# Optimization experiments

Measured on AMD Instinct MI355X. Metric: run time of the kernel, lower is better.

The kernel has to match this reference:

```python
import jax, jax.numpy as jnp
import numpy as np

DIM = 192
NUM_HEADS = 6
KSZ = 7
MLP_RATIO = 4.0
LEVELS = 8
EPS = 1e-5


def layernorm(x, w, b):
    mu = jnp.mean(x, axis=-1, keepdims=True)
    var = jnp.mean(jnp.square(x - mu), axis=-1, keepdims=True)
    return (x - mu) * jax.lax.rsqrt(var + EPS) * w + b


def na2d(x, qkv_w, qkv_b, proj_w, proj_b, rpb):
    # Neighborhood attention 2D with relative position bias (NATTEN semantics:
    # window of KSZ x KSZ keys per query, clamped to stay inside the image).
    B, H, W, C = x.shape
    nh, hd = NUM_HEADS, C // NUM_HEADS
    scale = hd ** -0.5
    qkv = (x @ qkv_w.T + qkv_b).reshape(B, H, W, 3, nh, hd)
    q = qkv[..., 0, :, :] * scale  # [B,H,W,nh,hd]
    k = qkv[..., 1, :, :]
    v = qkv[..., 2, :, :]

    si = jnp.clip(jnp.arange(H) - KSZ // 2, 0, H - KSZ)
    idx_i = si[:, None] + jnp.arange(KSZ)  # [H,KSZ] row indices of each window
    sj = jnp.clip(jnp.arange(W) - KSZ // 2, 0, W - KSZ)
    idx_j = sj[:, None] + jnp.arange(KSZ)  # [W,KSZ]

    def gather_win(t):  # [B,H,W,nh,hd] -> [B,H,KSZ,W,KSZ,nh,hd]
        t = jnp.take(t, idx_i.reshape(-1), axis=1).reshape(B, H, KSZ, W, nh, hd)
        t = jnp.take(t, idx_j.reshape(-1), axis=3).reshape(B, H, KSZ, W, KSZ, nh, hd)
        return t

    kw = gather_win(k)
    vw = gather_win(v)

    # scores over the KSZ x KSZ neighborhood
    scores = jnp.einsum('bxynd,bxiyjnd->bxynij', q, kw)  # [B,H,W,nh,KSZ,KSZ]

    # relative position bias: rpb is [nh, 2K-1, 2K-1]
    rel_i = idx_i - jnp.arange(H)[:, None] + (KSZ - 1)  # [H,KSZ] in [0,2K-2]
    rel_j = idx_j - jnp.arange(W)[:, None] + (KSZ - 1)  # [W,KSZ]
    bias = rpb[:, rel_i][:, :, :, rel_j]  # [nh,H,KSZ,W,KSZ]
    scores = scores + bias.transpose(1, 3, 0, 2, 4)[None]

    attn = jax.nn.softmax(scores.reshape(B, H, W, nh, KSZ * KSZ), axis=-1)
    attn = attn.reshape(B, H, W, nh, KSZ, KSZ)
    out = jnp.einsum('bxynij,bxiyjnd->bxynd', attn, vw).reshape(B, H, W, C)
    return out @ proj_w.T + proj_b


def setup_inputs() -> dict:
    key = jax.random.key(0)
    ks = jax.random.split(key, 8)
    C = DIM
    hidden = int(C * MLP_RATIO)
    init = lambda k, shape: (jax.random.normal(k, shape, dtype=jnp.float32) * 0.02)
    return {
        'x': jax.random.normal(ks[0], (1, 128, 128, C), dtype=jnp.float32),
        'qkv_w': init(ks[1], (3 * C, C)),
        'qkv_b': jnp.zeros((3 * C,), jnp.float32),
        'proj_w': init(ks[2], (C, C)),
        'proj_b': jnp.zeros((C,), jnp.float32),
        'rpb': init(ks[3], (NUM_HEADS, 2 * KSZ - 1, 2 * KSZ - 1)),
        'ln1_w': jnp.ones((C,), jnp.float32),
        'ln1_b': jnp.zeros((C,), jnp.float32),
        'ln2_w': jnp.ones((C,), jnp.float32),
        'ln2_b': jnp.zeros((C,), jnp.float32),
        'fc1_w': init(ks[4], (hidden, C)),
        'fc1_b': jnp.zeros((hidden,), jnp.float32),
        'fc2_w': init(ks[5], (C, hidden)),
        'fc2_b': jnp.zeros((C,), jnp.float32),
        'gamma1': jnp.ones((LEVELS, C), jnp.float32),
        'gamma2': jnp.ones((LEVELS, C), jnp.float32),
        'quality': 4,
    }


def reference(x, qkv_w, qkv_b, proj_w, proj_b, rpb, ln1_w, ln1_b, ln2_w, ln2_b,
              fc1_w, fc1_b, fc2_w, fc2_b, gamma1, gamma2, quality):
    # eval-mode quality gating; quality is an integer so l = quality % 1 == 0
    s = int(quality) - 1
    g1 = jnp.abs(gamma1[s])
    g2 = jnp.abs(gamma2[s])

    shortcut = x
    h = layernorm(x, ln1_w, ln1_b)
    a = na2d(h, qkv_w, qkv_b, proj_w, proj_b, rpb)
    x = shortcut + g1 * a
    h2 = layernorm(x, ln2_w, ln2_b)
    m = jax.nn.gelu(h2 @ fc1_w.T + fc1_b, approximate=False) @ fc2_w.T + fc2_b
    x = x + g2 * m
    return x
```

## Files before the change

kernel.cpp:

```cpp
#include <hip/hip_runtime.h>
#include <hip/hip_bf16.h>
#include <math.h>

#define DIM 192
#define NHD 6
#define HD 32
#define KSZ 7
#define HID 768
#define IMH 128
#define IMW 128
#define NPIX (IMH*IMW)
#define WIN 14
#define KPAD 40

typedef __attribute__((ext_vector_type(8))) short short8;
typedef __attribute__((ext_vector_type(4))) float f32x4;

#define LDS_SYNC() do { \
    asm volatile("s_waitcnt lgkmcnt(0)" ::: "memory"); \
    __builtin_amdgcn_sched_barrier(0); \
    __builtin_amdgcn_s_barrier(); } while (0)

__global__ __launch_bounds__(256) void cvt_w(
    const float* __restrict__ qw, __hip_bfloat16* __restrict__ dq)
{
    int idx = blockIdx.x * 1024 + threadIdx.x * 4;
    float4 v4 = *(const float4*)(qw + idx);
    union { ushort4 u; __hip_bfloat16 h[4]; } o;
    o.h[0] = __float2bfloat16(v4.x); o.h[1] = __float2bfloat16(v4.y);
    o.h[2] = __float2bfloat16(v4.z); o.h[3] = __float2bfloat16(v4.w);
    *(ushort4*)&dq[idx] = o.u;
}

__device__ __forceinline__ void gl_lds16(const void* g, void* l) {
    __builtin_amdgcn_global_load_lds(
        (const __attribute__((address_space(1))) void*)g,
        (__attribute__((address_space(3))) void*)l, 16, 0, 0);
}

__device__ __forceinline__ short8 cvt8(float4 a, float4 b) {
    union { short8 v; __hip_bfloat16 h[8]; } u;
    u.h[0] = __float2bfloat16(a.x); u.h[1] = __float2bfloat16(a.y);
    u.h[2] = __float2bfloat16(a.z); u.h[3] = __float2bfloat16(a.w);
    u.h[4] = __float2bfloat16(b.x); u.h[5] = __float2bfloat16(b.y);
    u.h[6] = __float2bfloat16(b.z); u.h[7] = __float2bfloat16(b.w);
    return u.v;
}

__device__ __forceinline__ void stage_rows(const __hip_bfloat16* __restrict__ src,
                                           char* ldsbase, int wave, int lane) {
    int c0 = wave * 96 + lane;
    int r0 = c0 / 24, k0 = c0 - r0 * 24;
    gl_lds16(src + (size_t)r0 * DIM + ((k0 ^ (r0 & 7)) * 8), ldsbase + (wave * 96) * 16);
    int c1 = wave * 96 + 64 + (lane & 31);
    int r1 = c1 / 24, k1 = c1 - r1 * 24;
    if (lane < 32)
        gl_lds16(src + (size_t)r1 * DIM + ((k1 ^ (r1 & 7)) * 8), ldsbase + (wave * 96 + 64) * 16);
}
__device__ __forceinline__ void stage_w2(const __hip_bfloat16* __restrict__ W2, int ch,
                                         char* ldsbase, int wave, int lane) {
    int i0 = wave * 96 + lane;
    int r0 = i0 >> 3, o0 = i0 & 7;
    gl_lds16(W2 + (size_t)r0 * HID + ch * 64 + ((o0 ^ (r0 & 7)) * 8), ldsbase + (wave * 96) * 16);
    int i1 = wave * 96 + 64 + (lane & 31);
    int r1 = i1 >> 3, o1 = i1 & 7;
    if (lane < 32)
        gl_lds16(W2 + (size_t)r1 * HID + ch * 64 + ((o1 ^ (r1 & 7)) * 8), ldsbase + (wave * 96 + 64) * 16);
}

__global__ __launch_bounds__(256, 2) void qkv_ln_gemm(
    const float* __restrict__ x, const float* __restrict__ lnw, const float* __restrict__ lnb,
    const __hip_bfloat16* __restrict__ W, const float* __restrict__ bias,
    float* __restrict__ qb, __hip_bfloat16* __restrict__ kb, __hip_bfloat16* __restrict__ vb)
{
    __shared__ __hip_bfloat16 As[32 * 192];
    __shared__ __hip_bfloat16 Ws2[2][64 * 192];
    int tid = threadIdx.x;
    int wave = tid >> 6, lane = tid & 63;
    int q = lane >> 4, col = lane & 15;
    int wm = (wave >> 1) * 16, wn = (wave & 1) * 32;
    int m0 = blockIdx.x * 32;

    auto stageW = [&](int ch, int buf) {
        #pragma unroll
        for (int i = 0; i < 6; i++) {
            int c = i * 256 + tid;
            int r = c / 24, kc = c - r * 24;
            gl_lds16(W + (size_t)(ch * 64 + r) * DIM + ((kc ^ (r & 7)) * 8),
                     (char*)&Ws2[buf][0] + (i * 256 + wave * 64) * 16);
        }
    };

    stageW(0, 0);

    {
        int row = tid >> 3, sub = tid & 7;
        const float4* xr = (const float4*)(x + (size_t)(m0 + row) * DIM + sub * 24);
        float4 xa[6];
        float s = 0.f;
        #pragma unroll
        for (int i = 0; i < 6; i++) {
            xa[i] = xr[i];
            s += xa[i].x + xa[i].y + xa[i].z + xa[i].w;
        }
        s += __shfl_xor(s, 1); s += __shfl_xor(s, 2); s += __shfl_xor(s, 4);
        float mu = s * (1.0f / DIM);
        float qs = 0.f;
        #pragma unroll
        for (int i = 0; i < 6; i++) {
            float a = xa[i].x - mu, b = xa[i].y - mu, c = xa[i].z - mu, d = xa[i].w - mu;
            qs += a * a + b * b + c * c + d * d;
        }
        qs += __shfl_xor(qs, 1); qs += __shfl_xor(qs, 2); qs += __shfl_xor(qs, 4);
        float rstd = rsqrtf(qs * (1.0f / DIM) + 1e-5f);
        const float4* wv = (const float4*)(lnw + sub * 24);
        const float4* bv = (const float4*)(lnb + sub * 24);
        #pragma unroll
        for (int j = 0; j < 3; j++) {
            float4 v0 = xa[j * 2], v1 = xa[j * 2 + 1];
            float4 w0 = wv[j * 2], w1 = wv[j * 2 + 1];
            float4 b0 = bv[j * 2], b1 = bv[j * 2 + 1];
            float4 o0, o1;
            o0.x = (v0.x - mu) * rstd * w0.x + b0.x;
            o0.y = (v0.y - mu) * rstd * w0.y + b0.y;
            o0.z = (v0.z - mu) * rstd * w0.z + b0.z;
            o0.w = (v0.w - mu) * rstd * w0.w + b0.w;
            o1.x = (v1.x - mu) * rstd * w1.x + b1.x;
            o1.y = (v1.y - mu) * rstd * w1.y + b1.y;
            o1.z = (v1.z - mu) * rstd * w1.z + b1.z;
            o1.w = (v1.w - mu) * rstd * w1.w + b1.w;
            int oct = sub * 3 + j;
            *(short8*)&As[row * 192 + ((oct ^ (row & 7)) * 8)] = cvt8(o0, o1);
        }
    }
    asm volatile("s_waitcnt lgkmcnt(0)" ::: "memory");
    __builtin_amdgcn_sched_barrier(0);
    __builtin_amdgcn_s_barrier();

    short8 af[6];
    {
        int rA = wm + col;
        #pragma unroll
        for (int ks = 0; ks < 6; ks++)
            af[ks] = *(const short8*)&As[rA * 192 + (((ks * 4 + q) ^ (rA & 7)) * 8)];
    }

    for (int ch = 0; ch < 9; ch++) {
        if (ch < 8) {
            stageW(ch + 1, (ch + 1) & 1);
            asm volatile("s_waitcnt vmcnt(6)" ::: "memory");
        } else {
            asm volatile("s_waitcnt vmcnt(0)" ::: "memory");
        }
        __builtin_amdgcn_s_barrier();
        const __hip_bfloat16* wsb = &Ws2[ch & 1][0];
        f32x4 acc[2] = {};
        #pragma unroll
        for (int ks = 0; ks < 6; ks++) {
            #pragma unroll
            for (int ni = 0; ni < 2; ni++) {
                int rB = wn + ni * 16 + col;
                short8 bf = *(const short8*)&wsb[rB * 192 + (((ks * 4 + q) ^ (rB & 7)) * 8)];
                acc[ni] = __builtin_amdgcn_mfma_f32_16x16x32_bf16(af[ks], bf, acc[ni], 0, 0, 0);
            }
        }
        #pragma unroll
        for (int ni = 0; ni < 2; ni++) {
            int n = ch * 64 + wn + ni * 16 + col;
            float bi = bias[n];
            int h18 = n >> 5;
            int sel = h18 / 6;
            int head = h18 - sel * 6;
            #pragma unroll
            for (int r4 = 0; r4 < 4; r4++) {
                int m = m0 + wm + q * 4 + r4;
                float v = acc[ni][r4] + bi;
                size_t idx = ((size_t)head * NPIX + m) * 32 + (n & 31);
                if (sel == 0)      qb[idx] = v * 0.17677669529663687f;
                else if (sel == 1) kb[idx] = __float2bfloat16(v);
                else               vb[idx] = __float2bfloat16(v);
            }
        }
        __builtin_amdgcn_s_barrier();
    }
}

__global__ __launch_bounds__(1024, 4) void tail_fused(
    const __hip_bfloat16* __restrict__ A, const __hip_bfloat16* __restrict__ Wp,
    const float* __restrict__ pb, const float* __restrict__ resid,
    const float* __restrict__ gamma1, const float* __restrict__ ln2w, const float* __restrict__ ln2b,
    const __hip_bfloat16* __restrict__ W1, const float* __restrict__ b1,
    const __hip_bfloat16* __restrict__ W2, const float* __restrict__ b2,
    const float* __restrict__ gamma2, const int* __restrict__ quality,
    float* __restrict__ outf)
{
    __shared__ __hip_bfloat16 arena[64 * 768];
    __shared__ __hip_bfloat16 Wsb[2][64 * 192];
    __shared__ float lnred[4][64][2];
    __hip_bfloat16* Hs = arena + 36864;

    int tid = threadIdx.x;
    int wave = tid >> 6, lane = tid & 63;
    int q = lane >> 4, col = lane & 15;
    int wm = (wave >> 2) * 16, wq4 = wave & 3;
    int m0 = blockIdx.x * 64;
    int s = quality[0] - 1;

    stage_rows(A + (size_t)m0 * DIM, (char*)Hs, wave, lane);
    stage_rows(Wp, (char*)&Wsb[0][0], wave, lane);
    stage_rows(Wp + 64 * DIM, (char*)&Wsb[1][0], wave, lane);
    asm volatile("s_waitcnt vmcnt(2)" ::: "memory");
    __builtin_amdgcn_s_barrier();

    short8 afp[6];
    {
        int rA = wm + col;
        #pragma unroll
        for (int ks = 0; ks < 6; ks++)
            afp[ks] = *(const short8*)&Hs[rA * 192 + (((ks * 4 + q) ^ (rA & 7)) * 8)];
    }

    float v[3][4];
    float sm[4] = {}, sq[4] = {};
    auto proj_chunk = [&](int ch, const __hip_bfloat16* wsb) {
        f32x4 pacc = {};
        int rB = wq4 * 16 + col;
        #pragma unroll
        for (int ks = 0; ks < 6; ks++) {
            short8 bf = *(const short8*)&wsb[rB * 192 + (((ks * 4 + q) ^ (rB & 7)) * 8)];
            pacc = __builtin_amdgcn_mfma_f32_16x16x32_bf16(afp[ks], bf, pacc, 0, 0, 0);
        }
        int n = ch * 64 + wq4 * 16 + col;
        float bi = pb[n];
        float g = fabsf(gamma1[s * DIM + n]);
        #pragma unroll
        for (int r = 0; r < 4; r++) {
            int m = m0 + wm + q * 4 + r;
            v[ch][r] = resid[(size_t)m * DIM + n] + g * (pacc[r] + bi);
            sm[r] += v[ch][r]; sq[r] += v[ch][r] * v[ch][r];
        }
    };

    proj_chunk(0, &Wsb[0][0]);
    __builtin_amdgcn_s_barrier();
    stage_rows(Wp + 128 * DIM, (char*)&Wsb[0][0], wave, lane);
    asm volatile("s_waitcnt vmcnt(2)" ::: "memory");
    __builtin_amdgcn_s_barrier();
    proj_chunk(1, &Wsb[1][0]);
    __builtin_amdgcn_s_barrier();
    stage_rows(W1, (char*)&Wsb[1][0], wave, lane);
    asm volatile("s_waitcnt vmcnt(2)" ::: "memory");
    __builtin_amdgcn_s_barrier();
    proj_chunk(2, &Wsb[0][0]);

    #pragma unroll
    for (int off = 1; off <= 8; off <<= 1)
        #pragma unroll
        for (int r = 0; r < 4; r++) {
            sm[r] += __shfl_xor(sm[r], off);
            sq[r] += __shfl_xor(sq[r], off);
        }
    if (col == 0) {
        #pragma unroll
        for (int r = 0; r < 4; r++) {
            lnred[wq4][wm + q * 4 + r][0] = sm[r];
            lnred[wq4][wm + q * 4 + r][1] = sq[r];
        }
    }
    LDS_SYNC();
    float mu[4], rstd[4];
    #pragma unroll
    for (int r = 0; r < 4; r++) {
        int ml = wm + q * 4 + r;
        float smt = lnred[0][ml][0] + lnred[1][ml][0] + lnred[2][ml][0] + lnred[3][ml][0];
        float sqt = lnred[0][ml][1] + lnred[1][ml][1] + lnred[2][ml][1] + lnred[3][ml][1];
        mu[r] = smt * (1.0f / DIM);
        float var = sqt * (1.0f / DIM) - mu[r] * mu[r];
        rstd[r] = rsqrtf(var + 1e-5f);
    }
    #pragma unroll
    for (int ch = 0; ch < 3; ch++) {
        int n = ch * 64 + wq4 * 16 + col;
        float lw = ln2w[n], lb = ln2b[n];
        #pragma unroll
        for (int r = 0; r < 4; r++) {
            int ml = wm + q * 4 + r;
            Hs[ml * 192 + (((n >> 3) ^ (ml & 7)) * 8) + (n & 7)] =
                __float2bfloat16((v[ch][r] - mu[r]) * rstd[r] * lw + lb);
        }
    }
    LDS_SYNC();
    short8 af1[6];
    {
        int rowA = wm + col;
        #pragma unroll
        for (int ks = 0; ks < 6; ks++)
            af1[ks] = *(const short8*)&Hs[rowA * 192 + (((ks * 4 + q) ^ (rowA & 7)) * 8)];
    }
    LDS_SYNC();

    for (int t = 0; t < 12; t++) {
        if (t < 11) stage_rows(W1 + (size_t)(t + 1) * 64 * DIM, (char*)&Wsb[t & 1][0], wave, lane);
        else        stage_w2(W2, 0, (char*)&Wsb[1][0], wave, lane);
        asm volatile("s_waitcnt vmcnt(2)" ::: "memory");
        __builtin_amdgcn_s_barrier();
        const __hip_bfloat16* wsb = &Wsb[(t + 1) & 1][0];
        f32x4 a1 = {};
        int rB = wq4 * 16 + col;
        #pragma unroll
        for (int ks = 0; ks < 6; ks++) {
            short8 bf = *(const short8*)&wsb[rB * 192 + (((ks * 4 + q) ^ (rB & 7)) * 8)];
            a1 = __builtin_amdgcn_mfma_f32_16x16x32_bf16(af1[ks], bf, a1, 0, 0, 0);
        }
        int n = t * 64 + wq4 * 16 + col;
        float bi = b1[n];
        int oct = n >> 3;
        #pragma unroll
        for (int r4 = 0; r4 < 4; r4++) {
            int row = wm + q * 4 + r4;
            float vv = a1[r4] + bi;
            float u = 0.7978845608f * (vv + 0.044715f * vv * vv * vv);
            float tt = 1.f - 2.f / (__expf(2.f * u) + 1.f);
            vv = 0.5f * vv * (1.f + tt);
            int osw = (oct & ~7) | ((oct ^ row) & 7);
            *(__hip_bfloat16*)((char*)arena + row * 1536 + osw * 16 + (n & 7) * 2) =
                __float2bfloat16(vv);
        }
        __builtin_amdgcn_s_barrier();
    }
    LDS_SYNC();

    f32x4 acc2[3] = {};
    for (int ch = 0; ch < 12; ch++) {
        if (ch < 11) {
            stage_w2(W2, ch + 1, (char*)&Wsb[ch & 1][0], wave, lane);
            asm volatile("s_waitcnt vmcnt(2)" ::: "memory");
        } else {
            asm volatile("s_waitcnt vmcnt(0)" ::: "memory");
        }
        __builtin_amdgcn_s_barrier();
        const __hip_bfloat16* wsb = &Wsb[(ch + 1) & 1][0];
        #pragma unroll
        for (int ks = 0; ks < 2; ks++) {
            int row = wm + col;
            int og = ch * 8 + ks * 4 + q;
            int osw = (og & ~7) | ((og ^ row) & 7);
            short8 a2 = *(const short8*)((char*)arena + row * 1536 + osw * 16);
            #pragma unroll
            for (int f = 0; f < 3; f++) {
                int rB = f * 64 + wq4 * 16 + col;
                short8 bf = *(const short8*)&wsb[rB * 64 + (((ks * 4 + q) ^ (rB & 7)) * 8)];
                acc2[f] = __builtin_amdgcn_mfma_f32_16x16x32_bf16(a2, bf, acc2[f], 0, 0, 0);
            }
        }
        __builtin_amdgcn_s_barrier();
    }

    #pragma unroll
    for (int f = 0; f < 3; f++) {
        int n = f * 64 + wq4 * 16 + col;
        float g = fabsf(gamma2[s * DIM + n]);
        float bi = b2[n];
        #pragma unroll
        for (int r4 = 0; r4 < 4; r4++) {
            int m = m0 + wm + q * 4 + r4;
            outf[(size_t)m * DIM + n] = v[f][r4] + g * (acc2[f][r4] + bi);
        }
    }
}

__device__ __forceinline__ void unpack8(const __hip_bfloat16* ptr, float* f) {
    short8 s8 = *(const short8*)ptr;
    union { short8 v; unsigned u[4]; } c; c.v = s8;
    #pragma unroll
    for (int w = 0; w < 4; w++) {
        f[2*w]   = __uint_as_float(c.u[w] << 16);
        f[2*w+1] = __uint_as_float(c.u[w] & 0xffff0000u);
    }
}

__global__ __launch_bounds__(256, 4) void attn_kernel3(
    const float* __restrict__ qbuf, const __hip_bfloat16* __restrict__ kbuf,
    const __hip_bfloat16* __restrict__ vbuf, const float* __restrict__ rpb,
    __hip_bfloat16* __restrict__ out,
    const float* __restrict__ pw, const float* __restrict__ f1w, const float* __restrict__ f2w,
    __hip_bfloat16* __restrict__ dp, __hip_bfloat16* __restrict__ df1, __hip_bfloat16* __restrict__ df2)
{
    if (blockIdx.x >= 256) {
        if (blockIdx.y != 0) return;
        int blk = blockIdx.x - 256, t = threadIdx.x;
        const float* s; __hip_bfloat16* d; int base;
        if (blk < 36)       { s = pw;  d = dp;  base = blk * 1024; }
        else if (blk < 180) { s = f1w; d = df1; base = (blk - 36) * 1024; }
        else                { s = f2w; d = df2; base = (blk - 180) * 1024; }
        int idx = base + t * 4;
        float4 v4 = *(const float4*)(s + idx);
        union { ushort4 u; __hip_bfloat16 h[4]; } o;
        o.h[0] = __float2bfloat16(v4.x); o.h[1] = __float2bfloat16(v4.y);
        o.h[2] = __float2bfloat16(v4.z); o.h[3] = __float2bfloat16(v4.w);
        *(ushort4*)&d[idx] = o.u;
        return;
    }

    __shared__ __hip_bfloat16 Ks[WIN * WIN * KPAD];
    __shared__ __hip_bfloat16 Vs[WIN * WIN * KPAD];
    __shared__ float rpbs[169];

    int head = blockIdx.y;
    int tile = blockIdx.x;
    int ti0 = (tile >> 4) * 8;
    int tj0 = (tile & 15) * 8;
    int wi0 = ti0 - 3; wi0 = wi0 < 0 ? 0 : (wi0 > IMH - WIN ? IMH - WIN : wi0);
    int wj0 = tj0 - 3; wj0 = wj0 < 0 ? 0 : (wj0 > IMW - WIN ? IMW - WIN : wj0);

    int tid = threadIdx.x;
    const size_t hbase = (size_t)head * NPIX;

    for (int c = tid; c < 784; c += 256) {
        int i = c / 56, part = c - i * 56;
        int n = i * WIN + (part >> 2);
        int dp2 = part & 3;
        size_t goff = (hbase + (size_t)(wi0 + i) * IMW + wj0) * 32 + part * 8;
        short8 kk = *(const short8*)(kbuf + goff);
        short8 vv = *(const short8*)(vbuf + goff);
        *(short8*)&Ks[n * KPAD + dp2 * 8] = kk;
        *(short8*)&Vs[n * KPAD + dp2 * 8] = vv;
    }
    if (tid < 169) rpbs[tid] = rpb[head * 169 + tid];

    int p   = tid >> 2;
    int sub = tid & 3;
    int pi = ti0 + (p >> 3), pj = tj0 + (p & 7);
    int si = pi - 3; si = si < 0 ? 0 : (si > IMH - KSZ ? IMH - KSZ : si);
    int sj = pj - 3; sj = sj < 0 ? 0 : (sj > IMW - KSZ ? IMW - KSZ : sj);
    int bi = si - wi0, bj = sj - wj0;

    const float4* qp = (const float4*)(qbuf + (hbase + (size_t)(pi * IMW + pj)) * 32 + sub * 8);
    float4 q0 = qp[0], q1 = qp[1];
    float q[8] = {q0.x, q0.y, q0.z, q0.w, q1.x, q1.y, q1.z, q1.w};

    __syncthreads();

    float m = -1e30f, l = 0.f;
    float acc[8] = {};
    #pragma unroll
    for (int ki = 0; ki < KSZ; ki++) {
        int rbase = (bi + ki) * WIN + bj;
        const float* rb = &rpbs[(si + ki - pi + 6) * 13 + (sj - pj + 6)];
        float s7[KSZ];
        #pragma unroll
        for (int kj = 0; kj < KSZ; kj++) {
            float kf[8];
            unpack8(&Ks[(rbase + kj) * KPAD + sub * 8], kf);
            float d = q[0]*kf[0] + q[1]*kf[1] + q[2]*kf[2] + q[3]*kf[3]
                    + q[4]*kf[4] + q[5]*kf[5] + q[6]*kf[6] + q[7]*kf[7];
            d += __shfl_xor(d, 1);
            d += __shfl_xor(d, 2);
            s7[kj] = d + rb[kj];
        }
        float rmax = s7[0];
        #pragma unroll
        for (int kj = 1; kj < KSZ; kj++) rmax = fmaxf(rmax, s7[kj]);
        float mn = fmaxf(m, rmax);
        float co = __expf(m - mn);
        l *= co;
        #pragma unroll
        for (int e = 0; e < 8; e++) acc[e] *= co;
        #pragma unroll
        for (int kj = 0; kj < KSZ; kj++) {
            float pw2 = __expf(s7[kj] - mn);
            l += pw2;
            float vf[8];
            unpack8(&Vs[(rbase + kj) * KPAD + sub * 8], vf);
            #pragma unroll
            for (int e = 0; e < 8; e++) acc[e] += pw2 * vf[e];
        }
        m = mn;
    }
    float rl = 1.f / l;
    __hip_bfloat16* op = out + (size_t)(pi * IMW + pj) * DIM + head * HD + sub * 8;
    #pragma unroll
    for (int e = 0; e < 8; e++) op[e] = __float2bfloat16(acc[e] * rl);
}

extern "C" void kernel_launch(void* const* d_in, const int* in_sizes, int n_in,
                              void* d_out, int out_size, void* d_ws, size_t ws_size,
                              hipStream_t stream)
{
    const float* x      = (const float*)d_in[0];
    const float* qkv_w  = (const float*)d_in[1];
    const float* qkv_b  = (const float*)d_in[2];
    const float* proj_w = (const float*)d_in[3];
    const float* proj_b = (const float*)d_in[4];
    const float* rpb    = (const float*)d_in[5];
    const float* ln1_w  = (const float*)d_in[6];
    const float* ln1_b  = (const float*)d_in[7];
    const float* ln2_w  = (const float*)d_in[8];
    const float* ln2_b  = (const float*)d_in[9];
    const float* fc1_w  = (const float*)d_in[10];
    const float* fc1_b  = (const float*)d_in[11];
    const float* fc2_w  = (const float*)d_in[12];
    const float* fc2_b  = (const float*)d_in[13];
    const float* gamma1 = (const float*)d_in[14];
    const float* gamma2 = (const float*)d_in[15];
    const int*   quality= (const int*)d_in[16];
    float* out = (float*)d_out;

    char* ws = (char*)d_ws;
    float*          qbuf   = (float*)ws;
    __hip_bfloat16* kbuf   = (__hip_bfloat16*)(ws + 12582912);
    __hip_bfloat16* vbuf   = (__hip_bfloat16*)(ws + 18874368);
    __hip_bfloat16* attn_b = (__hip_bfloat16*)(ws + 44040192);
    __hip_bfloat16* wq     = (__hip_bfloat16*)(ws + 50331648);
    __hip_bfloat16* wp     = (__hip_bfloat16*)(ws + 50552832);
    __hip_bfloat16* wf1    = (__hip_bfloat16*)(ws + 50626560);
    __hip_bfloat16* wf2    = (__hip_bfloat16*)(ws + 50921472);

    cvt_w<<<108, 256, 0, stream>>>(qkv_w, wq);
    qkv_ln_gemm<<<512, 256, 0, stream>>>(
        x, ln1_w, ln1_b, wq, qkv_b, qbuf, kbuf, vbuf);
    attn_kernel3<<<dim3(256 + 324, NHD), 256, 0, stream>>>(
        qbuf, kbuf, vbuf, rpb, attn_b, proj_w, fc1_w, fc2_w, wp, wf1, wf2);
    tail_fused<<<256, 1024, 0, stream>>>(
        attn_b, wp, proj_b, x, gamma1, ln2_w, ln2_b,
        wf1, fc1_b, wf2, fc2_b, gamma2, quality, out);
}
```

Before: 170.5 us.

## Fuse qkv weight conversion into GEMM and move other weight casts earlier

Removes the separate cvt_w launch by having qkv_ln_gemm load fp32 qkv weights into registers, convert them to bf16 and write them to LDS itself, with a register-staged double buffer in place of the direct global-to-LDS copies. The proj/fc1/fc2 weight conversion blocks move from the attention kernel to extra blocks appended to the qkv GEMM grid, so the attention grid no longer carries them. This saves a kernel launch, but every GEMM block now re-reads fp32 weights (twice the bytes) and spends VALU on conversion, and the extra registers for staging may lower occupancy.

```diff
diff --git a/kernel.cpp b/kernel.cpp
--- a/kernel.cpp
+++ b/kernel.cpp
@@ -21,17 +21,6 @@
     __builtin_amdgcn_sched_barrier(0); \
     __builtin_amdgcn_s_barrier(); } while (0)
 
-__global__ __launch_bounds__(256) void cvt_w(
-    const float* __restrict__ qw, __hip_bfloat16* __restrict__ dq)
-{
-    int idx = blockIdx.x * 1024 + threadIdx.x * 4;
-    float4 v4 = *(const float4*)(qw + idx);
-    union { ushort4 u; __hip_bfloat16 h[4]; } o;
-    o.h[0] = __float2bfloat16(v4.x); o.h[1] = __float2bfloat16(v4.y);
-    o.h[2] = __float2bfloat16(v4.z); o.h[3] = __float2bfloat16(v4.w);
-    *(ushort4*)&dq[idx] = o.u;
-}
-
 __device__ __forceinline__ void gl_lds16(const void* g, void* l) {
     __builtin_amdgcn_global_load_lds(
         (const __attribute__((address_space(1))) void*)g,
@@ -70,28 +59,55 @@
 
 __global__ __launch_bounds__(256, 2) void qkv_ln_gemm(
     const float* __restrict__ x, const float* __restrict__ lnw, const float* __restrict__ lnb,
-    const __hip_bfloat16* __restrict__ W, const float* __restrict__ bias,
-    float* __restrict__ qb, __hip_bfloat16* __restrict__ kb, __hip_bfloat16* __restrict__ vb)
+    const float* __restrict__ Wf, const float* __restrict__ bias,
+    float* __restrict__ qb, __hip_bfloat16* __restrict__ kb, __hip_bfloat16* __restrict__ vb,
+    const float* __restrict__ pw, const float* __restrict__ f1w, const float* __restrict__ f2w,
+    __hip_bfloat16* __restrict__ dp, __hip_bfloat16* __restrict__ df1, __hip_bfloat16* __restrict__ df2)
 {
     __shared__ __hip_bfloat16 As[32 * 192];
     __shared__ __hip_bfloat16 Ws2[2][64 * 192];
+
+    if (blockIdx.x >= 512) {
+        int blk = blockIdx.x - 512, t = threadIdx.x;
+        const float* s; __hip_bfloat16* d; int base;
+        if (blk < 36)       { s = pw;  d = dp;  base = blk * 1024; }
+        else if (blk < 180) { s = f1w; d = df1; base = (blk - 36) * 1024; }
+        else                { s = f2w; d = df2; base = (blk - 180) * 1024; }
+        int idx = base + t * 4;
+        float4 v4 = *(const float4*)(s + idx);
+        union { ushort4 u; __hip_bfloat16 h[4]; } o;
+        o.h[0] = __float2bfloat16(v4.x); o.h[1] = __float2bfloat16(v4.y);
+        o.h[2] = __float2bfloat16(v4.z); o.h[3] = __float2bfloat16(v4.w);
+        *(ushort4*)&d[idx] = o.u;
+        return;
+    }
+
     int tid = threadIdx.x;
     int wave = tid >> 6, lane = tid & 63;
     int q = lane >> 4, col = lane & 15;
     int wm = (wave >> 1) * 16, wn = (wave & 1) * 32;
     int m0 = blockIdx.x * 32;
 
-    auto stageW = [&](int ch, int buf) {
+    float4 wreg[12];
+    auto loadW = [&](int ch) {
         #pragma unroll
         for (int i = 0; i < 6; i++) {
             int c = i * 256 + tid;
             int r = c / 24, kc = c - r * 24;
-            gl_lds16(W + (size_t)(ch * 64 + r) * DIM + ((kc ^ (r & 7)) * 8),
-                     (char*)&Ws2[buf][0] + (i * 256 + wave * 64) * 16);
+            const float* src = Wf + (size_t)(ch * 64 + r) * DIM + ((kc ^ (r & 7)) * 8);
+            wreg[2 * i]     = *(const float4*)src;
+            wreg[2 * i + 1] = *(const float4*)(src + 4);
         }
     };
-
-    stageW(0, 0);
+    auto writeW = [&](int buf) {
+        #pragma unroll
+        for (int i = 0; i < 6; i++) {
+            int c = i * 256 + tid;
+            *(short8*)((char*)&Ws2[buf][0] + c * 16) = cvt8(wreg[2 * i], wreg[2 * i + 1]);
+        }
+    };
+
+    loadW(0);
 
     {
         int row = tid >> 3, sub = tid & 7;
@@ -133,6 +149,8 @@
             *(short8*)&As[row * 192 + ((oct ^ (row & 7)) * 8)] = cvt8(o0, o1);
         }
     }
+    asm volatile("s_waitcnt vmcnt(0)" ::: "memory");
+    writeW(0);
     asm volatile("s_waitcnt lgkmcnt(0)" ::: "memory");
     __builtin_amdgcn_sched_barrier(0);
     __builtin_amdgcn_s_barrier();
@@ -146,13 +164,7 @@
     }
 
     for (int ch = 0; ch < 9; ch++) {
-        if (ch < 8) {
-            stageW(ch + 1, (ch + 1) & 1);
-            asm volatile("s_waitcnt vmcnt(6)" ::: "memory");
-        } else {
-            asm volatile("s_waitcnt vmcnt(0)" ::: "memory");
-        }
-        __builtin_amdgcn_s_barrier();
+        if (ch < 8) loadW(ch + 1);
         const __hip_bfloat16* wsb = &Ws2[ch & 1][0];
         f32x4 acc[2] = {};
         #pragma unroll
@@ -163,6 +175,10 @@
                 short8 bf = *(const short8*)&wsb[rB * 192 + (((ks * 4 + q) ^ (rB & 7)) * 8)];
                 acc[ni] = __builtin_amdgcn_mfma_f32_16x16x32_bf16(af[ks], bf, acc[ni], 0, 0, 0);
             }
+        }
+        if (ch < 8) {
+            asm volatile("s_waitcnt vmcnt(0)" ::: "memory");
+            writeW((ch + 1) & 1);
         }
         #pragma unroll
         for (int ni = 0; ni < 2; ni++) {
@@ -181,7 +197,11 @@
                 else               vb[idx] = __float2bfloat16(v);
             }
         }
-        __builtin_amdgcn_s_barrier();
+        if (ch < 8) {
+            asm volatile("s_waitcnt lgkmcnt(0)" ::: "memory");
+            __builtin_amdgcn_sched_barrier(0);
+            __builtin_amdgcn_s_barrier();
+        }
     }
 }
 
@@ -382,26 +402,8 @@
 __global__ __launch_bounds__(256, 4) void attn_kernel3(
     const float* __restrict__ qbuf, const __hip_bfloat16* __restrict__ kbuf,
     const __hip_bfloat16* __restrict__ vbuf, const float* __restrict__ rpb,
-    __hip_bfloat16* __restrict__ out,
-    const float* __restrict__ pw, const float* __restrict__ f1w, const float* __restrict__ f2w,
-    __hip_bfloat16* __restrict__ dp, __hip_bfloat16* __restrict__ df1, __hip_bfloat16* __restrict__ df2)
+    __hip_bfloat16* __restrict__ out)
 {
-    if (blockIdx.x >= 256) {
-        if (blockIdx.y != 0) return;
-        int blk = blockIdx.x - 256, t = threadIdx.x;
-        const float* s; __hip_bfloat16* d; int base;
-        if (blk < 36)       { s = pw;  d = dp;  base = blk * 1024; }
-        else if (blk < 180) { s = f1w; d = df1; base = (blk - 36) * 1024; }
-        else                { s = f2w; d = df2; base = (blk - 180) * 1024; }
-        int idx = base + t * 4;
-        float4 v4 = *(const float4*)(s + idx);
-        union { ushort4 u; __hip_bfloat16 h[4]; } o;
-        o.h[0] = __float2bfloat16(v4.x); o.h[1] = __float2bfloat16(v4.y);
-        o.h[2] = __float2bfloat16(v4.z); o.h[3] = __float2bfloat16(v4.w);
-        *(ushort4*)&d[idx] = o.u;
-        return;
-    }
-
     __shared__ __hip_bfloat16 Ks[WIN * WIN * KPAD];
     __shared__ __hip_bfloat16 Vs[WIN * WIN * KPAD];
     __shared__ float rpbs[169];
@@ -511,16 +513,14 @@
     __hip_bfloat16* kbuf   = (__hip_bfloat16*)(ws + 12582912);
     __hip_bfloat16* vbuf   = (__hip_bfloat16*)(ws + 18874368);
     __hip_bfloat16* attn_b = (__hip_bfloat16*)(ws + 44040192);
-    __hip_bfloat16* wq     = (__hip_bfloat16*)(ws + 50331648);
     __hip_bfloat16* wp     = (__hip_bfloat16*)(ws + 50552832);
     __hip_bfloat16* wf1    = (__hip_bfloat16*)(ws + 50626560);
     __hip_bfloat16* wf2    = (__hip_bfloat16*)(ws + 50921472);
 
-    cvt_w<<<108, 256, 0, stream>>>(qkv_w, wq);
-    qkv_ln_gemm<<<512, 256, 0, stream>>>(
-        x, ln1_w, ln1_b, wq, qkv_b, qbuf, kbuf, vbuf);
-    attn_kernel3<<<dim3(256 + 324, NHD), 256, 0, stream>>>(
-        qbuf, kbuf, vbuf, rpb, attn_b, proj_w, fc1_w, fc2_w, wp, wf1, wf2);
+    qkv_ln_gemm<<<512 + 324, 256, 0, stream>>>(
+        x, ln1_w, ln1_b, qkv_w, qkv_b, qbuf, kbuf, vbuf,
+        proj_w, fc1_w, fc2_w, wp, wf1, wf2);
+    attn_kernel3<<<dim3(256, NHD), 256, 0, stream>>>(qbuf, kbuf, vbuf, rpb, attn_b);
     tail_fused<<<256, 1024, 0, stream>>>(
         attn_b, wp, proj_b, x, gamma1, ln2_w, ln2_b,
         wf1, fc1_b, wf2, fc2_b, gamma2, quality, out);
```

New measurement: 172.0 us. No clear change (+0.9%).
